# Optimization experiments

Hardware: AMD Instinct MI355X
Metric: run time of the kernel (lower is better)

## Reference

```python
import jax, jax.numpy as jnp
import numpy as np


def setup_inputs() -> dict:
    key = jax.random.key(0)
    ks = jax.random.split(key, 4)
    B, S, D, H, E = 4, 2048, 1024, 4096, 4
    sd = 1.0 / np.sqrt(D)
    sh = 1.0 / np.sqrt(H)
    return {
        "x": jax.random.normal(ks[0], (B, S, D), jnp.float32),
        "Wr": jax.random.normal(ks[1], (D, E), jnp.float32) * sd,
        "W1": jax.random.normal(ks[2], (E, D, H), jnp.float32) * sd,
        "b1": jnp.zeros((E, H), jnp.float32),
        "W2": jax.random.normal(ks[3], (E, H, D), jnp.float32) * sh,
        "b2": jnp.zeros((E, D), jnp.float32),
        "top_k": 2,
    }


def reference(x, Wr, W1, b1, W2, b2, top_k):
    # Router: softmax over experts, then top-k + renormalize (as in torch code)
    logits = jnp.einsum("bsd,de->bse", x, Wr)              # [B,S,E]
    probs = jax.nn.softmax(logits, axis=-1)
    wk, idx = jax.lax.top_k(probs, top_k)                  # [B,S,K]
    wk = wk / jnp.sum(wk, axis=-1, keepdims=True)
    # Scatter top-k weights back to dense per-expert weights [B,S,E]
    E = probs.shape[-1]
    onehot = jax.nn.one_hot(idx, E, dtype=x.dtype)         # [B,S,K,E]
    weights = jnp.einsum("bsk,bske->bse", wk, onehot)      # [B,S,E]
    # Expert MLPs (Linear-ReLU-Linear), computed dense over experts and
    # combined with the (mostly-zero) routing weights — same math as the
    # gather/scatter loop in the torch module.
    h = jax.nn.relu(jnp.einsum("bsd,edh->bseh", x, W1) + b1)   # [B,S,E,H]
    y = jnp.einsum("bseh,ehd->bsed", h, W2) + b2               # [B,S,E,D]
    out = jnp.einsum("bse,bsed->bsd", weights, y)              # [B,S,D]
    aux_loss = jnp.asarray(0.0, dtype=x.dtype)
    return out, aux_loss
```

## Files before the change

### kernel.cpp

```cpp
#include <hip/hip_runtime.h>
#include <cstdint>
#include <cstddef>

typedef _Float16 f16;
typedef __attribute__((ext_vector_type(8))) f16 f16x8;
typedef __attribute__((ext_vector_type(4))) f16 f16x4;
typedef __attribute__((ext_vector_type(4))) float f32x4;

#define M_TOK 8192
#define DDIM 1024
#define HDIM 4096
#define NEXP 4
#define TOTPAD 16896

__device__ __forceinline__ void async_copy16(const void* g, void* s) {
    __builtin_amdgcn_global_load_lds((__attribute__((address_space(1))) void*)g,
                                     (__attribute__((address_space(3))) void*)s,
                                     16, 0, 0);
}

__global__ __launch_bounds__(256) void router_kernel(
    const float* __restrict__ x, const float* __restrict__ Wr,
    float* __restrict__ wts, int* __restrict__ top2, float2* __restrict__ wpair) {
    __shared__ float wr_s[DDIM * NEXP];
    for (int i = threadIdx.x; i < DDIM * NEXP; i += 256) wr_s[i] = Wr[i];
    __syncthreads();
    const int wave = threadIdx.x >> 6, lane = threadIdx.x & 63;
    const int t = blockIdx.x * 4 + wave;
    float a0 = 0.f, a1 = 0.f, a2 = 0.f, a3 = 0.f;
    const float* xr = x + (size_t)t * DDIM;
    for (int i = 0; i < DDIM; i += 256) {
        const int d = i + lane * 4;
        const float4 v = *(const float4*)(xr + d);
        const float* w0 = &wr_s[d * 4];
        a0 += v.x * w0[0] + v.y * w0[4] + v.z * w0[8]  + v.w * w0[12];
        a1 += v.x * w0[1] + v.y * w0[5] + v.z * w0[9]  + v.w * w0[13];
        a2 += v.x * w0[2] + v.y * w0[6] + v.z * w0[10] + v.w * w0[14];
        a3 += v.x * w0[3] + v.y * w0[7] + v.z * w0[11] + v.w * w0[15];
    }
    for (int off = 32; off > 0; off >>= 1) {
        a0 += __shfl_xor(a0, off, 64);
        a1 += __shfl_xor(a1, off, 64);
        a2 += __shfl_xor(a2, off, 64);
        a3 += __shfl_xor(a3, off, 64);
    }
    if (lane == 0) {
        float lg[4] = {a0, a1, a2, a3};
        int i1 = 0;
        for (int e = 1; e < 4; ++e) if (lg[e] > lg[i1]) i1 = e;
        int i2 = -1;
        for (int e = 0; e < 4; ++e) {
            if (e == i1) continue;
            if (i2 < 0 || lg[e] > lg[i2]) i2 = e;
        }
        const float w1 = 1.0f / (1.0f + expf(lg[i2] - lg[i1]));
        float w[4] = {0.f, 0.f, 0.f, 0.f};
        w[i1] = w1; w[i2] = 1.0f - w1;
        float* o = wts + (size_t)t * 4;
        o[0] = w[0]; o[1] = w[1]; o[2] = w[2]; o[3] = w[3];
        top2[t] = i1 | (i2 << 8);
        wpair[t] = make_float2(w1, 1.0f - w1);
    }
}

__global__ __launch_bounds__(256) void count_kernel(
    const int* __restrict__ top2, int* __restrict__ meta) {
    __shared__ int lc[4];
    if (threadIdx.x < 4) lc[threadIdx.x] = 0;
    __syncthreads();
    const int t = blockIdx.x * 256 + threadIdx.x;
    const int p = top2[t];
    atomicAdd(&lc[p & 0xff], 1);
    atomicAdd(&lc[(p >> 8) & 0xff], 1);
    __syncthreads();
    if (threadIdx.x < 4) atomicAdd(&meta[threadIdx.x], lc[threadIdx.x]);
}

__global__ void offsets_kernel(int* __restrict__ meta) {
    if (threadIdx.x == 0) {
        int off = 0;
        for (int e = 0; e < 4; ++e) {
            const int c = meta[e];
            const int cp = (c + 127) & ~127;
            meta[4 + e] = cp;
            meta[8 + e] = off;
            off += cp;
        }
    }
}

__global__ __launch_bounds__(256) void fill_kernel(
    const int* __restrict__ top2, int* __restrict__ meta,
    int* __restrict__ toklist, int2* __restrict__ slotmap) {
    __shared__ int lc[4], base[4];
    if (threadIdx.x < 4) lc[threadIdx.x] = 0;
    __syncthreads();
    const int t = blockIdx.x * 256 + threadIdx.x;
    const int p = top2[t];
    const int e1 = p & 0xff, e2 = (p >> 8) & 0xff;
    const int r1 = atomicAdd(&lc[e1], 1);
    const int r2 = atomicAdd(&lc[e2], 1);
    __syncthreads();
    if (threadIdx.x < 4) base[threadIdx.x] = atomicAdd(&meta[12 + threadIdx.x], lc[threadIdx.x]);
    __syncthreads();
    const int p1 = meta[8 + e1] + base[e1] + r1;
    const int p2 = meta[8 + e2] + base[e2] + r2;
    toklist[p1] = t;
    toklist[p2] = t;
    slotmap[t] = make_int2(p1, p2);
}

__global__ __launch_bounds__(256) void convert_f16_kernel(
    const float* __restrict__ in, f16* __restrict__ out, int n4) {
    const int i = blockIdx.x * 256 + threadIdx.x;
    if (i < n4) {
        const float4 v = ((const float4*)in)[i];
        f16x4 o = {(f16)v.x, (f16)v.y, (f16)v.z, (f16)v.w};
        ((f16x4*)out)[i] = o;
    }
}

__global__ __launch_bounds__(256) void pack_b_kernel(
    const float* __restrict__ in0, f16* __restrict__ out0, int K, int N) {
    __shared__ float tile[64][65];
    const float* in = in0 + (size_t)blockIdx.z * K * N;
    f16* out = out0 + (size_t)blockIdx.z * K * N;
    const int n0 = blockIdx.x * 64, k0 = blockIdx.y * 64;
    const int tx = threadIdx.x & 63, ty = threadIdx.x >> 6;
#pragma unroll
    for (int i = 0; i < 64; i += 4)
        tile[ty + i][tx] = in[(size_t)(k0 + ty + i) * N + n0 + tx];
    __syncthreads();
#pragma unroll
    for (int c = 0; c < 2; ++c) {
        const int cc = c * 256 + threadIdx.x;
        const int grp = cc >> 7;
        const int within = cc & 127;
        const int kk2 = within >> 6, quad = (within >> 4) & 3, l16 = within & 15;
        const int nl = grp * 16 + l16;
        const int kl = kk2 * 32 + quad * 8;
        f16x8 v;
#pragma unroll
        for (int j = 0; j < 8; ++j) v[j] = (f16)tile[kl + j][nl];
        const size_t o = ((size_t)(n0 / 16 + grp) * (K >> 6) + (k0 >> 6)) * 1024 +
                         (size_t)within * 8;
        *(f16x8*)&out[o] = v;
    }
}

template <int MODE>
__global__ __launch_bounds__(256, 3) void gemm_kernel(
    const f16* __restrict__ A, const f16* __restrict__ Bswz,
    int N, int K,
    const float* __restrict__ bias,
    f16* __restrict__ outH, float* __restrict__ outF,
    const float* __restrict__ wts,
    const int* __restrict__ toklist, const int* __restrict__ meta, int e0) {
    __shared__ __align__(16) f16 As[2][128 * 64];
    const int zz = blockIdx.z;
    const int e = e0 + zz;
    const int m0 = blockIdx.x * 128, n0 = blockIdx.y * 128;

    int cnt = M_TOK, off = 0;
    if (meta) {
        cnt = meta[e];
        const int cp = meta[4 + e];
        off = meta[8 + e];
        if (m0 >= cp) return;
    }

    const f16* Be = Bswz + (size_t)zz * N * K;
    const float* be = bias + (size_t)zz * N;

    const int tid = threadIdx.x;
    const int wave = tid >> 6, lane = tid & 63;
    const int wm = wave >> 1, wn = wave & 1;
    const int quad = lane >> 4, l16 = lane & 15;
    const int Kb = K >> 6;

    f32x4 acc[4][4] = {};

    const int lrb = tid >> 3;
    const int gcoff = (((tid & 7) ^ (lrb & 7)) * 8);
    const f16* ga[4];
#pragma unroll
    for (int r = 0; r < 4; ++r) {
        const int gm = m0 + r * 32 + lrb;
        int arow;
        if (MODE == 0) arow = toklist ? toklist[off + gm] : gm;
        else arow = off + gm;
        ga[r] = A + (size_t)arow * K + gcoff;
    }

    const f16* bp[4];
#pragma unroll
    for (int j = 0; j < 4; ++j)
        bp[j] = Be + ((size_t)(n0 / 16 + wn * 4 + j) * Kb) * 1024 + lane * 8;

#pragma unroll
    for (int r = 0; r < 4; ++r)
        async_copy16(ga[r], &As[0][(r * 256 + tid) * 8]);
    __syncthreads();

    const int swl = l16 & 7;
    int p = 0;
    for (int k0b = 0; k0b < Kb; ++k0b) {
        f16x8 bf[2][4];
#pragma unroll
        for (int kk2 = 0; kk2 < 2; ++kk2)
#pragma unroll
            for (int j = 0; j < 4; ++j)
                bf[kk2][j] = *(const f16x8*)(bp[j] + (k0b << 10) + (kk2 << 9));

        if (k0b + 1 < Kb) {
            const int kn = (k0b + 1) << 6;
#pragma unroll
            for (int r = 0; r < 4; ++r)
                async_copy16(ga[r] + kn, &As[p ^ 1][(r * 256 + tid) * 8]);
        }

#pragma unroll
        for (int kk2 = 0; kk2 < 2; ++kk2) {
            f16x8 af[4];
#pragma unroll
            for (int i = 0; i < 4; ++i)
                af[i] = *(const f16x8*)&As[p][(size_t)(wm * 64 + i * 16 + l16) * 64 +
                                             (((kk2 * 4 + quad) ^ swl) << 3)];
#pragma unroll
            for (int i = 0; i < 4; ++i)
#pragma unroll
                for (int j = 0; j < 4; ++j)
                    acc[i][j] = __builtin_amdgcn_mfma_f32_16x16x32_f16(af[i], bf[kk2][j], acc[i][j], 0, 0, 0);
        }
        __syncthreads();
        p ^= 1;
    }

#pragma unroll
    for (int i = 0; i < 4; ++i) {
        const int mbase = m0 + wm * 64 + i * 16 + quad * 4;
#pragma unroll
        for (int j = 0; j < 4; ++j) {
            const int n = n0 + wn * 64 + j * 16 + l16;
            const float bv = be[n];
#pragma unroll
            for (int r = 0; r < 4; ++r) {
                const int m = mbase + r;
                float v = acc[i][j][r] + bv;
                if (MODE == 0) {
                    v = v > 0.0f ? v : 0.0f;
                    outH[(size_t)(off + m) * N + n] = (f16)v;
                } else {
                    if (outH) {
                        outH[(size_t)(off + m) * N + n] = (f16)v;
                    } else if (m < cnt) {
                        const float w = wts[m * 4 + e];
                        atomicAdd(&outF[(size_t)m * N + n], w * v);
                    }
                }
            }
        }
    }
}

__global__ __launch_bounds__(256) void combine_kernel(
    const f16* __restrict__ yseg, const int2* __restrict__ slotmap,
    const float2* __restrict__ wpair, float* __restrict__ out, int aux_idx) {
    const int t = blockIdx.x;
    const int2 p = slotmap[t];
    const float2 w = wpair[t];
    const int d = threadIdx.x * 4;
    const f16x4 a = *(const f16x4*)&yseg[(size_t)p.x * DDIM + d];
    const f16x4 b = *(const f16x4*)&yseg[(size_t)p.y * DDIM + d];
    float4 o;
    o.x = w.x * (float)a[0] + w.y * (float)b[0];
    o.y = w.x * (float)a[1] + w.y * (float)b[1];
    o.z = w.x * (float)a[2] + w.y * (float)b[2];
    o.w = w.x * (float)a[3] + w.y * (float)b[3];
    *(float4*)&out[(size_t)t * DDIM + d] = o;
    if (t == 0 && threadIdx.x == 0 && aux_idx >= 0) out[aux_idx] = 0.0f;
}

extern "C" void kernel_launch(void* const* d_in, const int* in_sizes, int n_in,
                              void* d_out, int out_size, void* d_ws, size_t ws_size,
                              hipStream_t stream) {
    (void)in_sizes; (void)n_in;
    const float* x  = (const float*)d_in[0];
    const float* Wr = (const float*)d_in[1];
    const float* W1 = (const float*)d_in[2];
    const float* b1 = (const float*)d_in[3];
    const float* W2 = (const float*)d_in[4];
    const float* b2 = (const float*)d_in[5];
    float* out = (float*)d_out;

    char* ws = (char*)d_ws;
    float*  wts   = (float*)ws;
    int*    meta  = (int*)(ws + (128 << 10));
    int*    top2  = (int*)(ws + (132 << 10));
    int*    tokl  = (int*)(ws + (164 << 10));
    float2* wpair = (float2*)(ws + (240 << 10));
    int2*   slotm = (int2*)(ws + (304 << 10));
    f16*    xb    = (f16*)(ws + (512 << 10));
    const size_t MBs = 1ull << 20;
    const size_t base = (512 << 10) + 16 * MBs;

    const size_t SPARSE_NEED = (512 << 10) + 80 * MBs + (size_t)TOTPAD * HDIM * sizeof(f16);
    const bool sparse = ws_size >= SPARSE_NEED;

    const int aux_idx = (out_size == M_TOK * DDIM + 1) ? (M_TOK * DDIM) : -1;

    f16 *w1t, *w2t, *h, *yseg;
    if (sparse) {
        w1t  = (f16*)(ws + base);
        w2t  = (f16*)(ws + base + 32 * MBs);
        h    = (f16*)(ws + base + 64 * MBs);
        yseg = (f16*)(ws + (512 << 10));
    } else {
        w1t = (f16*)(ws + base);
        w2t = (f16*)(ws + base + 8 * MBs);
        h   = (f16*)(ws + base + 16 * MBs);
        yseg = nullptr;
    }

    router_kernel<<<M_TOK / 4, 256, 0, stream>>>(x, Wr, wts, top2, wpair);
    convert_f16_kernel<<<(M_TOK * DDIM / 4) / 256, 256, 0, stream>>>(x, xb, M_TOK * DDIM / 4);

    if (sparse) {
        hipMemsetAsync(meta, 0, 16 * sizeof(int), stream);
        hipMemsetAsync(tokl, 0, (size_t)TOTPAD * sizeof(int), stream);
        count_kernel<<<M_TOK / 256, 256, 0, stream>>>(top2, meta);
        offsets_kernel<<<1, 64, 0, stream>>>(meta);
        fill_kernel<<<M_TOK / 256, 256, 0, stream>>>(top2, meta, tokl, slotm);
        pack_b_kernel<<<dim3(HDIM / 64, DDIM / 64, NEXP), 256, 0, stream>>>(W1, w1t, DDIM, HDIM);
        pack_b_kernel<<<dim3(DDIM / 64, HDIM / 64, NEXP), 256, 0, stream>>>(W2, w2t, HDIM, DDIM);
        gemm_kernel<0><<<dim3(M_TOK / 128, HDIM / 128, NEXP), 256, 0, stream>>>(
            xb, w1t, HDIM, DDIM, b1, h, nullptr, wts, tokl, meta, 0);
        gemm_kernel<1><<<dim3(M_TOK / 128, DDIM / 128, NEXP), 256, 0, stream>>>(
            h, w2t, DDIM, HDIM, b2, yseg, nullptr, wts, tokl, meta, 0);
        combine_kernel<<<M_TOK, 256, 0, stream>>>(yseg, slotm, wpair, out, aux_idx);
    } else {
        hipMemsetAsync(out, 0, (size_t)out_size * sizeof(float), stream);
        for (int e = 0; e < NEXP; ++e) {
            pack_b_kernel<<<dim3(HDIM / 64, DDIM / 64, 1), 256, 0, stream>>>(
                W1 + (size_t)e * DDIM * HDIM, w1t, DDIM, HDIM);
            gemm_kernel<0><<<dim3(M_TOK / 128, HDIM / 128, 1), 256, 0, stream>>>(
                xb, w1t, HDIM, DDIM, b1 + (size_t)e * HDIM, h, nullptr, wts, nullptr, nullptr, e);
            pack_b_kernel<<<dim3(DDIM / 64, HDIM / 64, 1), 256, 0, stream>>>(
                W2 + (size_t)e * HDIM * DDIM, w2t, HDIM, DDIM);
            gemm_kernel<1><<<dim3(M_TOK / 128, DDIM / 128, 1), 256, 0, stream>>>(
                h, w2t, DDIM, HDIM, b2 + (size_t)e * DDIM, nullptr, out, wts, nullptr, nullptr, e);
        }
    }
}
```

Measured before the change: 684.0 us.

## Rework MoE GEMMs with 256-row tiles, split-K atomics and fused conversion

The router now also writes the fp16 copy of x, so the separate conversion kernel is gone. The grouped GEMM moves to 256x128 tiles with a deeper async LDS pipeline that uses explicit ds_read_b128, waitcnt and setprio control. The second GEMM is split along K in two halves and scatter-adds weighted results straight into the output, which removes the combine kernel and the intermediate fp16 buffer. Segment padding grows to 256 rows, adding wasted compute on padding, and the float atomics and extra output memset add traffic while making the summation order non-deterministic.

```diff
diff --git a/kernel.cpp b/kernel.cpp
--- a/kernel.cpp
+++ b/kernel.cpp
@@ -11,7 +11,7 @@
 #define DDIM 1024
 #define HDIM 4096
 #define NEXP 4
-#define TOTPAD 16896
+#define TOTPAD 17408
 
 __device__ __forceinline__ void async_copy16(const void* g, void* s) {
     __builtin_amdgcn_global_load_lds((__attribute__((address_space(1))) void*)g,
@@ -19,9 +19,25 @@
                                      16, 0, 0);
 }
 
+__device__ __forceinline__ f16x8 ds_read_b128_f16(uint32_t addr) {
+    f16x8 r;
+    asm volatile("ds_read_b128 %0, %1" : "=v"(r) : "v"(addr));
+    return r;
+}
+__device__ __forceinline__ uint32_t lds_addr(const void* p) {
+    return (uint32_t)(uintptr_t)(__attribute__((address_space(3))) const void*)p;
+}
+
+__device__ __forceinline__ void stageA(const f16* const* ga, int koff,
+                                       f16* plane, int tid) {
+#pragma unroll
+    for (int g = 0; g < 4; ++g)
+        async_copy16(ga[g] + koff, plane + g * 2048 + tid * 8);
+}
+
 __global__ __launch_bounds__(256) void router_kernel(
     const float* __restrict__ x, const float* __restrict__ Wr,
-    float* __restrict__ wts, int* __restrict__ top2, float2* __restrict__ wpair) {
+    float* __restrict__ wts, int* __restrict__ top2, f16* __restrict__ xb) {
     __shared__ float wr_s[DDIM * NEXP];
     for (int i = threadIdx.x; i < DDIM * NEXP; i += 256) wr_s[i] = Wr[i];
     __syncthreads();
@@ -29,9 +45,12 @@
     const int t = blockIdx.x * 4 + wave;
     float a0 = 0.f, a1 = 0.f, a2 = 0.f, a3 = 0.f;
     const float* xr = x + (size_t)t * DDIM;
+    f16* xo = xb + (size_t)t * DDIM;
     for (int i = 0; i < DDIM; i += 256) {
         const int d = i + lane * 4;
         const float4 v = *(const float4*)(xr + d);
+        f16x4 o = {(f16)v.x, (f16)v.y, (f16)v.z, (f16)v.w};
+        *(f16x4*)(xo + d) = o;
         const float* w0 = &wr_s[d * 4];
         a0 += v.x * w0[0] + v.y * w0[4] + v.z * w0[8]  + v.w * w0[12];
         a1 += v.x * w0[1] + v.y * w0[5] + v.z * w0[9]  + v.w * w0[13];
@@ -59,7 +78,6 @@
         float* o = wts + (size_t)t * 4;
         o[0] = w[0]; o[1] = w[1]; o[2] = w[2]; o[3] = w[3];
         top2[t] = i1 | (i2 << 8);
-        wpair[t] = make_float2(w1, 1.0f - w1);
     }
 }
 
@@ -81,7 +99,7 @@
         int off = 0;
         for (int e = 0; e < 4; ++e) {
             const int c = meta[e];
-            const int cp = (c + 127) & ~127;
+            const int cp = (c + 255) & ~255;
             meta[4 + e] = cp;
             meta[8 + e] = off;
             off += cp;
@@ -91,7 +109,7 @@
 
 __global__ __launch_bounds__(256) void fill_kernel(
     const int* __restrict__ top2, int* __restrict__ meta,
-    int* __restrict__ toklist, int2* __restrict__ slotmap) {
+    int* __restrict__ toklist) {
     __shared__ int lc[4], base[4];
     if (threadIdx.x < 4) lc[threadIdx.x] = 0;
     __syncthreads();
@@ -103,21 +121,8 @@
     __syncthreads();
     if (threadIdx.x < 4) base[threadIdx.x] = atomicAdd(&meta[12 + threadIdx.x], lc[threadIdx.x]);
     __syncthreads();
-    const int p1 = meta[8 + e1] + base[e1] + r1;
-    const int p2 = meta[8 + e2] + base[e2] + r2;
-    toklist[p1] = t;
-    toklist[p2] = t;
-    slotmap[t] = make_int2(p1, p2);
-}
-
-__global__ __launch_bounds__(256) void convert_f16_kernel(
-    const float* __restrict__ in, f16* __restrict__ out, int n4) {
-    const int i = blockIdx.x * 256 + threadIdx.x;
-    if (i < n4) {
-        const float4 v = ((const float4*)in)[i];
-        f16x4 o = {(f16)v.x, (f16)v.y, (f16)v.z, (f16)v.w};
-        ((f16x4*)out)[i] = o;
-    }
+    toklist[meta[8 + e1] + base[e1] + r1] = t;
+    toklist[meta[8 + e2] + base[e2] + r2] = t;
 }
 
 __global__ __launch_bounds__(256) void pack_b_kernel(
@@ -148,137 +153,134 @@
     }
 }
 
-template <int MODE>
-__global__ __launch_bounds__(256, 3) void gemm_kernel(
-    const f16* __restrict__ A, const f16* __restrict__ Bswz,
-    int N, int K,
-    const float* __restrict__ bias,
-    f16* __restrict__ outH, float* __restrict__ outF,
-    const float* __restrict__ wts,
-    const int* __restrict__ toklist, const int* __restrict__ meta, int e0) {
-    __shared__ __align__(16) f16 As[2][128 * 64];
-    const int zz = blockIdx.z;
+template <int MODE, int SPLIT>
+__global__ __launch_bounds__(256, 2) void gemm_kernel(
+    const f16* __restrict__ A, const f16* __restrict__ Bf, int N, int K,
+    const float* __restrict__ bias, f16* __restrict__ outH, float* __restrict__ outF,
+    const float* __restrict__ wts, const int* __restrict__ toklist,
+    const int* __restrict__ meta, int e0) {
+    __shared__ __align__(16) f16 S[2][16384];
+    const int zz = blockIdx.z / SPLIT, kh = blockIdx.z % SPLIT;
     const int e = e0 + zz;
-    const int m0 = blockIdx.x * 128, n0 = blockIdx.y * 128;
-
-    int cnt = M_TOK, off = 0;
-    if (meta) {
-        cnt = meta[e];
-        const int cp = meta[4 + e];
-        off = meta[8 + e];
-        if (m0 >= cp) return;
-    }
-
-    const f16* Be = Bswz + (size_t)zz * N * K;
+    const int m0 = blockIdx.x * 256, n0 = blockIdx.y * 128;
+    int cnt = M_TOK, cp = M_TOK, off = 0;
+    if (meta) { cnt = meta[e]; cp = meta[4 + e]; off = meta[8 + e]; }
+    if (m0 >= cp) return;
+
+    const int Kb = K >> 6;
+    const int NT = (K / SPLIT) >> 6;
+    const int kb0 = kh * NT;
+
+    const f16* Be = Bf + (size_t)zz * N * K;
     const float* be = bias + (size_t)zz * N;
 
     const int tid = threadIdx.x;
     const int wave = tid >> 6, lane = tid & 63;
     const int wm = wave >> 1, wn = wave & 1;
     const int quad = lane >> 4, l16 = lane & 15;
-    const int Kb = K >> 6;
-
-    f32x4 acc[4][4] = {};
-
-    const int lrb = tid >> 3;
-    const int gcoff = (((tid & 7) ^ (lrb & 7)) * 8);
+
+    const int r0 = tid >> 2;
+    const int gswz = ((tid & 3) ^ ((r0 >> 1) & 3)) * 8;
     const f16* ga[4];
 #pragma unroll
-    for (int r = 0; r < 4; ++r) {
-        const int gm = m0 + r * 32 + lrb;
+    for (int g = 0; g < 4; ++g) {
+        const int gm = m0 + g * 64 + r0;
         int arow;
         if (MODE == 0) arow = toklist ? toklist[off + gm] : gm;
         else arow = off + gm;
-        ga[r] = A + (size_t)arow * K + gcoff;
-    }
-
+        ga[g] = A + (size_t)arow * K + (size_t)kb0 * 64 + gswz;
+    }
     const f16* bp[4];
 #pragma unroll
     for (int j = 0; j < 4; ++j)
         bp[j] = Be + ((size_t)(n0 / 16 + wn * 4 + j) * Kb) * 1024 + lane * 8;
 
-#pragma unroll
-    for (int r = 0; r < 4; ++r)
-        async_copy16(ga[r], &As[0][(r * 256 + tid) * 8]);
-    __syncthreads();
-
-    const int swl = l16 & 7;
+    const int chq = ((quad ^ ((l16 >> 1) & 3)) << 3);
+    const uint32_t sb0 = lds_addr(&S[0][0]), sb1 = lds_addr(&S[1][0]);
+    const uint32_t a_b = (uint32_t)(((wm * 128 + l16) * 32 + chq) * 2);
+
+    f32x4 acc[8][4] = {};
+
+    stageA(ga, 0,  S[0] + 0,    tid);
+    stageA(ga, 32, S[0] + 8192, tid);
+    if (NT > 1) {
+        stageA(ga, 64, S[1] + 0, tid);
+        asm volatile("s_waitcnt vmcnt(4)" ::: "memory");
+    } else {
+        asm volatile("s_waitcnt vmcnt(0)" ::: "memory");
+    }
+    __builtin_amdgcn_s_barrier();
+
     int p = 0;
-    for (int k0b = 0; k0b < Kb; ++k0b) {
-        f16x8 bf[2][4];
-#pragma unroll
-        for (int kk2 = 0; kk2 < 2; ++kk2)
+#pragma unroll 1
+    for (int t = 0; t < NT; ++t) {
+        const uint32_t sp = p ? sb1 : sb0;
+        f16* SpW = S[p];
+        f16* SoW = S[p ^ 1];
+        f16x8 af[8], bfv[4];
+#pragma unroll
+        for (int j = 0; j < 4; ++j)
+            bfv[j] = *(const f16x8*)(bp[j] + ((size_t)(kb0 + t) << 10));
+#pragma unroll
+        for (int i = 0; i < 8; ++i) af[i] = ds_read_b128_f16(sp + a_b + i * 1024);
+        if (t + 1 < NT) stageA(ga, ((t + 1) << 6) + 32, SoW + 8192, tid);
+        __builtin_amdgcn_s_barrier();
+        asm volatile("s_waitcnt lgkmcnt(0)" ::: "memory");
+        __builtin_amdgcn_sched_barrier(0);
+        __builtin_amdgcn_s_setprio(1);
+#pragma unroll
+        for (int i = 0; i < 8; ++i)
 #pragma unroll
             for (int j = 0; j < 4; ++j)
-                bf[kk2][j] = *(const f16x8*)(bp[j] + (k0b << 10) + (kk2 << 9));
-
-        if (k0b + 1 < Kb) {
-            const int kn = (k0b + 1) << 6;
-#pragma unroll
-            for (int r = 0; r < 4; ++r)
-                async_copy16(ga[r] + kn, &As[p ^ 1][(r * 256 + tid) * 8]);
-        }
-
-#pragma unroll
-        for (int kk2 = 0; kk2 < 2; ++kk2) {
-            f16x8 af[4];
-#pragma unroll
-            for (int i = 0; i < 4; ++i)
-                af[i] = *(const f16x8*)&As[p][(size_t)(wm * 64 + i * 16 + l16) * 64 +
-                                             (((kk2 * 4 + quad) ^ swl) << 3)];
-#pragma unroll
-            for (int i = 0; i < 4; ++i)
-#pragma unroll
-                for (int j = 0; j < 4; ++j)
-                    acc[i][j] = __builtin_amdgcn_mfma_f32_16x16x32_f16(af[i], bf[kk2][j], acc[i][j], 0, 0, 0);
-        }
-        __syncthreads();
+                acc[i][j] = __builtin_amdgcn_mfma_f32_16x16x32_f16(af[i], bfv[j], acc[i][j], 0, 0, 0);
+        __builtin_amdgcn_s_setprio(0);
+        __builtin_amdgcn_s_barrier();
+#pragma unroll
+        for (int j = 0; j < 4; ++j)
+            bfv[j] = *(const f16x8*)(bp[j] + ((size_t)(kb0 + t) << 10) + 512);
+#pragma unroll
+        for (int i = 0; i < 8; ++i)
+            af[i] = ds_read_b128_f16(sp + a_b + 16384 + i * 1024);
+        if (t + 2 < NT) stageA(ga, (t + 2) << 6, SpW, tid);
+        __builtin_amdgcn_s_barrier();
+        asm volatile("s_waitcnt lgkmcnt(0)" ::: "memory");
+        __builtin_amdgcn_sched_barrier(0);
+        __builtin_amdgcn_s_setprio(1);
+#pragma unroll
+        for (int i = 0; i < 8; ++i)
+#pragma unroll
+            for (int j = 0; j < 4; ++j)
+                acc[i][j] = __builtin_amdgcn_mfma_f32_16x16x32_f16(af[i], bfv[j], acc[i][j], 0, 0, 0);
+        __builtin_amdgcn_s_setprio(0);
+        if (t + 1 < NT) {
+            if (t + 2 < NT) asm volatile("s_waitcnt vmcnt(8)" ::: "memory");
+            else            asm volatile("s_waitcnt vmcnt(4)" ::: "memory");
+            __builtin_amdgcn_s_barrier();
+        }
         p ^= 1;
     }
 
 #pragma unroll
-    for (int i = 0; i < 4; ++i) {
-        const int mbase = m0 + wm * 64 + i * 16 + quad * 4;
+    for (int i = 0; i < 8; ++i) {
+        const int mb = m0 + wm * 128 + i * 16 + quad * 4;
 #pragma unroll
         for (int j = 0; j < 4; ++j) {
             const int n = n0 + wn * 64 + j * 16 + l16;
-            const float bv = be[n];
+            const float bv = (MODE == 0 || kh == 0) ? be[n] : 0.0f;
 #pragma unroll
             for (int r = 0; r < 4; ++r) {
-                const int m = mbase + r;
+                const int m = mb + r;
                 float v = acc[i][j][r] + bv;
                 if (MODE == 0) {
                     v = v > 0.0f ? v : 0.0f;
                     outH[(size_t)(off + m) * N + n] = (f16)v;
-                } else {
-                    if (outH) {
-                        outH[(size_t)(off + m) * N + n] = (f16)v;
-                    } else if (m < cnt) {
-                        const float w = wts[m * 4 + e];
-                        atomicAdd(&outF[(size_t)m * N + n], w * v);
-                    }
+                } else if (m < cnt) {
+                    const int tok = toklist ? toklist[off + m] : m;
+                    atomicAdd(&outF[(size_t)tok * N + n], wts[tok * 4 + e] * v);
                 }
             }
         }
     }
-}
-
-__global__ __launch_bounds__(256) void combine_kernel(
-    const f16* __restrict__ yseg, const int2* __restrict__ slotmap,
-    const float2* __restrict__ wpair, float* __restrict__ out, int aux_idx) {
-    const int t = blockIdx.x;
-    const int2 p = slotmap[t];
-    const float2 w = wpair[t];
-    const int d = threadIdx.x * 4;
-    const f16x4 a = *(const f16x4*)&yseg[(size_t)p.x * DDIM + d];
-    const f16x4 b = *(const f16x4*)&yseg[(size_t)p.y * DDIM + d];
-    float4 o;
-    o.x = w.x * (float)a[0] + w.y * (float)b[0];
-    o.y = w.x * (float)a[1] + w.y * (float)b[1];
-    o.z = w.x * (float)a[2] + w.y * (float)b[2];
-    o.w = w.x * (float)a[3] + w.y * (float)b[3];
-    *(float4*)&out[(size_t)t * DDIM + d] = o;
-    if (t == 0 && threadIdx.x == 0 && aux_idx >= 0) out[aux_idx] = 0.0f;
 }
 
 extern "C" void kernel_launch(void* const* d_in, const int* in_sizes, int n_in,
@@ -298,8 +300,6 @@
     int*    meta  = (int*)(ws + (128 << 10));
     int*    top2  = (int*)(ws + (132 << 10));
     int*    tokl  = (int*)(ws + (164 << 10));
-    float2* wpair = (float2*)(ws + (240 << 10));
-    int2*   slotm = (int2*)(ws + (304 << 10));
     f16*    xb    = (f16*)(ws + (512 << 10));
     const size_t MBs = 1ull << 20;
     const size_t base = (512 << 10) + 16 * MBs;
@@ -307,47 +307,42 @@
     const size_t SPARSE_NEED = (512 << 10) + 80 * MBs + (size_t)TOTPAD * HDIM * sizeof(f16);
     const bool sparse = ws_size >= SPARSE_NEED;
 
-    const int aux_idx = (out_size == M_TOK * DDIM + 1) ? (M_TOK * DDIM) : -1;
-
-    f16 *w1t, *w2t, *h, *yseg;
+    f16 *w1t, *w2t, *h;
     if (sparse) {
-        w1t  = (f16*)(ws + base);
-        w2t  = (f16*)(ws + base + 32 * MBs);
-        h    = (f16*)(ws + base + 64 * MBs);
-        yseg = (f16*)(ws + (512 << 10));
+        w1t = (f16*)(ws + base);
+        w2t = (f16*)(ws + base + 32 * MBs);
+        h   = (f16*)(ws + base + 64 * MBs);
     } else {
         w1t = (f16*)(ws + base);
         w2t = (f16*)(ws + base + 8 * MBs);
         h   = (f16*)(ws + base + 16 * MBs);
-        yseg = nullptr;
-    }
-
-    router_kernel<<<M_TOK / 4, 256, 0, stream>>>(x, Wr, wts, top2, wpair);
-    convert_f16_kernel<<<(M_TOK * DDIM / 4) / 256, 256, 0, stream>>>(x, xb, M_TOK * DDIM / 4);
+    }
+
+    router_kernel<<<M_TOK / 4, 256, 0, stream>>>(x, Wr, wts, top2, xb);
+    hipMemsetAsync(out, 0, (size_t)out_size * sizeof(float), stream);
 
     if (sparse) {
         hipMemsetAsync(meta, 0, 16 * sizeof(int), stream);
         hipMemsetAsync(tokl, 0, (size_t)TOTPAD * sizeof(int), stream);
         count_kernel<<<M_TOK / 256, 256, 0, stream>>>(top2, meta);
         offsets_kernel<<<1, 64, 0, stream>>>(meta);
-        fill_kernel<<<M_TOK / 256, 256, 0, stream>>>(top2, meta, tokl, slotm);
+        fill_kernel<<<M_TOK / 256, 256, 0, stream>>>(top2, meta, tokl);
         pack_b_kernel<<<dim3(HDIM / 64, DDIM / 64, NEXP), 256, 0, stream>>>(W1, w1t, DDIM, HDIM);
         pack_b_kernel<<<dim3(DDIM / 64, HDIM / 64, NEXP), 256, 0, stream>>>(W2, w2t, HDIM, DDIM);
-        gemm_kernel<0><<<dim3(M_TOK / 128, HDIM / 128, NEXP), 256, 0, stream>>>(
+        const int GX = TOTPAD / 256;
+        gemm_kernel<0, 1><<<dim3(GX, HDIM / 128, NEXP), 256, 0, stream>>>(
             xb, w1t, HDIM, DDIM, b1, h, nullptr, wts, tokl, meta, 0);
-        gemm_kernel<1><<<dim3(M_TOK / 128, DDIM / 128, NEXP), 256, 0, stream>>>(
-            h, w2t, DDIM, HDIM, b2, yseg, nullptr, wts, tokl, meta, 0);
-        combine_kernel<<<M_TOK, 256, 0, stream>>>(yseg, slotm, wpair, out, aux_idx);
+        gemm_kernel<1, 2><<<dim3(GX, DDIM / 128, NEXP * 2), 256, 0, stream>>>(
+            h, w2t, DDIM, HDIM, b2, nullptr, out, wts, tokl, meta, 0);
     } else {
-        hipMemsetAsync(out, 0, (size_t)out_size * sizeof(float), stream);
         for (int e = 0; e < NEXP; ++e) {
             pack_b_kernel<<<dim3(HDIM / 64, DDIM / 64, 1), 256, 0, stream>>>(
                 W1 + (size_t)e * DDIM * HDIM, w1t, DDIM, HDIM);
-            gemm_kernel<0><<<dim3(M_TOK / 128, HDIM / 128, 1), 256, 0, stream>>>(
+            gemm_kernel<0, 1><<<dim3(M_TOK / 256, HDIM / 128, 1), 256, 0, stream>>>(
                 xb, w1t, HDIM, DDIM, b1 + (size_t)e * HDIM, h, nullptr, wts, nullptr, nullptr, e);
             pack_b_kernel<<<dim3(DDIM / 64, HDIM / 64, 1), 256, 0, stream>>>(
                 W2 + (size_t)e * HDIM * DDIM, w2t, HDIM, DDIM);
-            gemm_kernel<1><<<dim3(M_TOK / 128, DDIM / 128, 1), 256, 0, stream>>>(
+            gemm_kernel<1, 1><<<dim3(M_TOK / 256, DDIM / 128, 1), 256, 0, stream>>>(
                 h, w2t, DDIM, HDIM, b2 + (size_t)e * DDIM, nullptr, out, wts, nullptr, nullptr, e);
         }
     }
```

After: 880.4 us. 1.29x slower.
